# Kernel optimization log

Hardware: AMD Instinct MI355X
Metric: run time of the kernel (lower is better)

Reference implementation:

```python
import jax, jax.numpy as jnp
import numpy as np

IB = 8      # input/hidden activation bits
ABMVM = 8   # gate activation bits after MVM
ABNM = 8    # near-memory compute bits
NL = 0.05   # analog noise level
CY_DIV = 2.0
CY_SCALE = 2.0


def quant_pass(x, wb, sign):
    # Faithful port of QuantFunc.forward: clip/clamp then fake-quant (round to grid).
    if wb is None or wb == 0:
        return x
    if sign:
        delta = 0.0 if wb == 1 else 1.0 / (2.0 ** (wb - 1))
        x = jnp.clip(x, -1.0 + delta, 1.0 - delta)
    else:
        x = jnp.clip(x, 0.0, 1.0)
    if wb == 1:
        return jnp.sign(x)
    scale = 2.0 ** (wb - 1) if sign else 2.0 ** wb
    return jnp.round(x * scale) / scale


def setup_inputs() -> dict:
    key = jax.random.key(0)
    ks = jax.random.split(key, 7)
    B, I, H = 4096, 1024, 1024
    return {
        "input": jax.random.normal(ks[0], (B, I), jnp.float32),
        "hx": jax.random.normal(ks[1], (B, H), jnp.float32),
        "cx": jax.random.normal(ks[2], (B, H), jnp.float32),
        "weight_ih": jax.random.normal(ks[3], (4 * H, I), jnp.float32) * 0.1,
        "weight_hh": jax.random.normal(ks[4], (4 * H, H), jnp.float32) * 0.1,
        "bias_ih": jax.random.normal(ks[5], (4 * H,), jnp.float32) * 0.1,
        "bias_hh": jax.random.normal(ks[6], (4 * H,), jnp.float32) * 0.1,
        "train": 0,
    }


def reference(input, hx, cx, weight_ih, weight_hh, bias_ih, bias_hh, train):
    # Per-call Gaussian noise (simulated analog hardware); fixed key for reproducibility.
    nk = jax.random.split(jax.random.key(42), 4)
    noise_w_ih = jax.random.normal(nk[0], weight_ih.T.shape, weight_ih.dtype) * weight_ih.max() * NL
    noise_w_hh = jax.random.normal(nk[1], weight_hh.T.shape, weight_hh.dtype) * weight_hh.max() * NL
    noise_b_ih = jax.random.normal(nk[2], bias_ih.shape, bias_ih.dtype) * bias_ih.max() * NL
    noise_b_hh = jax.random.normal(nk[3], bias_hh.shape, bias_hh.dtype) * bias_hh.max() * NL

    # gates: [B, 4H]
    gates = (quant_pass(input, IB, True) @ (weight_ih.T + noise_w_ih) + bias_ih + noise_b_ih
             + quant_pass(hx, IB, True) @ (weight_hh.T + noise_w_hh) + bias_hh + noise_b_hh)

    ingate, forgetgate, cellgate, outgate = jnp.split(gates, 4, axis=1)
    ingate = quant_pass(jax.nn.sigmoid(ingate), ABMVM, False)
    forgetgate = quant_pass(jax.nn.sigmoid(forgetgate), ABMVM, False)
    cellgate = quant_pass(jnp.tanh(cellgate), ABMVM, True)
    outgate = quant_pass(jax.nn.sigmoid(outgate), ABMVM, False)

    cy = quant_pass((quant_pass(forgetgate * cx, ABNM, True)
                     + quant_pass(ingate * cellgate, ABNM, True)) / CY_DIV, ABNM, True)
    hy = quant_pass(outgate * quant_pass(jnp.tanh(cy * CY_SCALE), ABNM, True), ABNM, True)
    return (hy, cy)
```

## Files before the change

### kernel.cpp

```cpp
#include <hip/hip_runtime.h>
#include <hip/hip_bf16.h>
#include <stdint.h>
#include <stddef.h>


#define PART 1

typedef __attribute__((ext_vector_type(8))) short bf16x8;
typedef __attribute__((ext_vector_type(4))) float f32x4;

#define BATCH 4096

#define WS_A_OFF    ((size_t)0)
#define WS_B_OFF    ((size_t)16 << 20)
#define WS_G_OFF    ((size_t)48 << 20)
#define WS_BIAS_OFF ((size_t)112 << 20)
#define WS_MAX_OFF  (WS_BIAS_OFF + 16384)

__host__ __device__ inline void tf2x32(uint32_t k0, uint32_t k1,
                                       uint32_t x0, uint32_t x1,
                                       uint32_t &o0, uint32_t &o1)
{
  const uint32_t k2 = k0 ^ k1 ^ 0x1BD11BDAu;
#define TFR(r) { x0 += x1; x1 = (x1 << (r)) | (x1 >> (32 - (r))); x1 ^= x0; }
  x0 += k0; x1 += k1;
  TFR(13) TFR(15) TFR(26) TFR(6)
  x0 += k1; x1 += k2 + 1u;
  TFR(17) TFR(29) TFR(16) TFR(24)
  x0 += k2; x1 += k0 + 2u;
  TFR(13) TFR(15) TFR(26) TFR(6)
  x0 += k0; x1 += k1 + 3u;
  TFR(17) TFR(29) TFR(16) TFR(24)
  x0 += k1; x1 += k2 + 4u;
  TFR(13) TFR(15) TFR(26) TFR(6)
  x0 += k2; x1 += k0 + 5u;
#undef TFR
  o0 = x0; o1 = x1;
}

__device__ inline uint32_t jax_bits32(uint32_t k0, uint32_t k1, uint32_t i, uint32_t size)
{
#if PART
  uint32_t a, b;
  tf2x32(k0, k1, 0u, i, a, b);
  return a ^ b;
#else
  uint32_t half = size >> 1, a, b;
  if (i < half) { tf2x32(k0, k1, i, i + half, a, b); return a; }
  tf2x32(k0, k1, i - half, i, a, b); return b;
#endif
}

__device__ inline float bits_to_normal(uint32_t bits)
{
  float f = __uint_as_float((bits >> 9) | 0x3F800000u) - 1.0f;
  const float lo = -0x1.fffffep-1f;
  float u = fmaxf(lo, f * 2.0f + lo);
  float w = -log1pf(-u * u);
  float p;
  if (w < 5.0f) {
    w -= 2.5f;
    p = 2.81022636e-08f;
    p = fmaf(p, w, 3.43273939e-07f);
    p = fmaf(p, w, -3.5233877e-06f);
    p = fmaf(p, w, -4.39150654e-06f);
    p = fmaf(p, w, 0.00021858087f);
    p = fmaf(p, w, -0.00125372503f);
    p = fmaf(p, w, -0.00417768164f);
    p = fmaf(p, w, 0.246640727f);
    p = fmaf(p, w, 1.50140941f);
  } else {
    w = sqrtf(w) - 3.0f;
    p = -0.000200214257f;
    p = fmaf(p, w, 0.000100950558f);
    p = fmaf(p, w, 0.00134934322f);
    p = fmaf(p, w, -0.00367342844f);
    p = fmaf(p, w, 0.00573950773f);
    p = fmaf(p, w, -0.0076224613f);
    p = fmaf(p, w, 0.00943887047f);
    p = fmaf(p, w, 1.00167406f);
    p = fmaf(p, w, 2.83297682f);
  }
  return 0x1.6a09e6p+0f * (p * u);
}

__device__ inline float quantS8(float x)
{
  x = fminf(fmaxf(x, -0.9921875f), 0.9921875f);
  return rintf(x * 128.0f) * 0.0078125f;
}
__device__ inline float quantU8(float x)
{
  x = fminf(fmaxf(x, 0.0f), 1.0f);
  return rintf(x * 256.0f) * 0.00390625f;
}
__device__ inline float sigmoid_xla(float x) { return 0.5f + 0.5f * tanhf(0.5f * x); }

__device__ inline unsigned short f2bf(float x)
{
  uint32_t b = __float_as_uint(x);
  return (unsigned short)((b + 0x7FFFu + ((b >> 16) & 1u)) >> 16);
}
__device__ inline float bf2f(unsigned short u) { return __uint_as_float(((uint32_t)u) << 16); }

__device__ inline float dec_max(uint32_t u)
{
  uint32_t bits = (u & 0x80000000u) ? (u ^ 0x80000000u) : ~u;
  return __uint_as_float(bits);
}

__global__ void init_max(uint32_t* mx)
{
  if (threadIdx.x < 4) mx[threadIdx.x] = 0u;
}

__global__ void kmax(const float4* __restrict__ a, int n4, uint32_t* __restrict__ out)
{
  float m = -3.4e38f;
  for (int i = blockIdx.x * blockDim.x + threadIdx.x; i < n4; i += gridDim.x * blockDim.x) {
    float4 v = a[i];
    m = fmaxf(fmaxf(m, fmaxf(v.x, v.y)), fmaxf(v.z, v.w));
  }
  for (int off = 32; off; off >>= 1) m = fmaxf(m, __shfl_down(m, off, 64));
  __shared__ float sm[4];
  if ((threadIdx.x & 63) == 0) sm[threadIdx.x >> 6] = m;
  __syncthreads();
  if (threadIdx.x == 0) {
    float bm = sm[0];
    for (int w = 1; w < (int)(blockDim.x >> 6); ++w) bm = fmaxf(bm, sm[w]);
    uint32_t bits = __float_as_uint(bm);
    uint32_t enc = (bits & 0x80000000u) ? ~bits : (bits | 0x80000000u);
    atomicMax(out, enc);
  }
}

__global__ void build_A(const float4* __restrict__ in, const float4* __restrict__ hx,
                        unsigned short* __restrict__ A)
{
  int t = blockIdx.x * 256 + threadIdx.x;
  int b = t >> 9;
  int kq = t & 511;
  float4 v = (kq < 256) ? in[b * 256 + kq] : hx[b * 256 + (kq - 256)];
  unsigned short o[4];
  o[0] = f2bf(quantS8(v.x)); o[1] = f2bf(quantS8(v.y));
  o[2] = f2bf(quantS8(v.z)); o[3] = f2bf(quantS8(v.w));
  *reinterpret_cast<uint64_t*>(A + (size_t)t * 4) = *reinterpret_cast<uint64_t*>(o);
}

__global__ void build_B(const float* __restrict__ wih, const float* __restrict__ whh,
                        unsigned short* __restrict__ B, const uint32_t* __restrict__ mxenc,
                        uint32_t kih0, uint32_t kih1, uint32_t khh0, uint32_t khh1)
{
  uint32_t t = blockIdx.x * 256u + threadIdx.x;
  uint32_t arr = t >> 22;
  uint32_t r = t & 4194303u;
  uint32_t k = r & 1023u;
  uint32_t n = r >> 10;
  const float* w = arr ? whh : wih;
  float mx = dec_max(mxenc[arr]);
  uint32_t key0 = arr ? khh0 : kih0, key1 = arr ? khh1 : kih1;
  uint32_t i = k * 4096u + n;
  float nrm = bits_to_normal(jax_bits32(key0, key1, i, 4194304u));
  float weff = w[(size_t)n * 1024u + k] + (nrm * mx) * 0.05f;
  unsigned short hi = f2bf(weff);
  unsigned short lob = f2bf(weff - bf2f(hi));
  size_t base = (size_t)n * 4096u + (arr ? 1024u : 0u) + k;
  B[base] = hi;
  B[base + 2048u] = lob;
}

__global__ void build_bias(const float* __restrict__ bih, const float* __restrict__ bhh,
                           float* __restrict__ biasE, const uint32_t* __restrict__ mxenc,
                           uint32_t kbi0, uint32_t kbi1, uint32_t kbh0, uint32_t kbh1)
{
  uint32_t j = blockIdx.x * 256u + threadIdx.x;
  if (j >= 4096u) return;
  float mi = dec_max(mxenc[2]), mh = dec_max(mxenc[3]);
  float ni = (bits_to_normal(jax_bits32(kbi0, kbi1, j, 4096u)) * mi) * 0.05f;
  float nh = (bits_to_normal(jax_bits32(kbh0, kbh1, j, 4096u)) * mh) * 0.05f;
  biasE[j] = ((bih[j] + ni) + bhh[j]) + nh;
}


__device__ __forceinline__ void gload_lds16(const void* g, void* l)
{
  __builtin_amdgcn_global_load_lds((__attribute__((address_space(1))) void*)g,
                                   (__attribute__((address_space(3))) void*)l, 16, 0, 0);
}

#define VM4  asm volatile("s_waitcnt vmcnt(4)" ::: "memory")
#define VM0  asm volatile("s_waitcnt vmcnt(0)" ::: "memory")
#define NOVM

#define TILE_ONE(t_, DO_STAGE_, VM_ASM_)                                          \
  {                                                                               \
    const int buf_ = (t_) & 3;                                                    \
    const unsigned char* pa_ = lds + buf_ * 32768 + aoff;                         \
    const unsigned char* pb_ = lds + buf_ * 32768 + boff;                         \
    bf16x8 bfr_[4], af_[4];                                                       \
    _Pragma("unroll") for (int n_ = 0; n_ < 4; ++n_)                              \
      bfr_[n_] = *(const bf16x8*)(pb_ + n_ * 1024);                               \
    _Pragma("unroll") for (int m_ = 0; m_ < 4; ++m_)                              \
      af_[m_] = *(const bf16x8*)(pa_ + m_ * 1024);                                \
    if (DO_STAGE_) {                                                              \
      const int ts_ = (t_) + 2;                                                   \
      unsigned char* la_ = lds + (ts_ & 3) * 32768;                               \
      const int ka_ = (ts_ * 32) & 2047;                                          \
      gload_lds16(Ar0 + ka_, la_ + tid * 16);                                     \
      gload_lds16(Ar1 + ka_, la_ + 8192 + tid * 16);                              \
    }                                                                             \
    __builtin_amdgcn_s_barrier();                                                 \
    __builtin_amdgcn_sched_barrier(0);                                            \
    __builtin_amdgcn_s_setprio(1);                                                \
    _Pragma("unroll") for (int m_ = 0; m_ < 4; ++m_)                              \
      _Pragma("unroll") for (int n_ = 0; n_ < 4; ++n_)                            \
        acc[m_][n_] = __builtin_amdgcn_mfma_f32_16x16x32_bf16(af_[m_], bfr_[n_],  \
                                                              acc[m_][n_], 0, 0, 0); \
    __builtin_amdgcn_s_setprio(0);                                                \
    __builtin_amdgcn_s_barrier();                                                 \
    __builtin_amdgcn_sched_barrier(0);                                            \
    _Pragma("unroll") for (int m_ = 0; m_ < 4; ++m_)                              \
      af_[m_] = *(const bf16x8*)(pa_ + (4 + m_) * 1024);                          \
    if (DO_STAGE_) {                                                              \
      const int ts_ = (t_) + 2;                                                   \
      unsigned char* lb_ = lds + (ts_ & 3) * 32768 + 16384;                       \
      const size_t kb_ = (size_t)ts_ * 32;                                        \
      gload_lds16(Br0 + kb_, lb_ + tid * 16);                                     \
      gload_lds16(Br1 + kb_, lb_ + 8192 + tid * 16);                              \
    }                                                                             \
    __builtin_amdgcn_s_barrier();                                                 \
    __builtin_amdgcn_sched_barrier(0);                                            \
    __builtin_amdgcn_s_setprio(1);                                                \
    _Pragma("unroll") for (int m_ = 0; m_ < 4; ++m_)                              \
      _Pragma("unroll") for (int n_ = 0; n_ < 4; ++n_)                            \
        acc[4 + m_][n_] = __builtin_amdgcn_mfma_f32_16x16x32_bf16(af_[m_], bfr_[n_], \
                                                              acc[4 + m_][n_], 0, 0, 0); \
    __builtin_amdgcn_s_setprio(0);                                                \
    VM_ASM_;                                                                      \
    __builtin_amdgcn_s_barrier();                                                 \
    __builtin_amdgcn_sched_barrier(0);                                            \
  }

__global__ __launch_bounds__(512, 2) void gemm_gates(
    const unsigned short* __restrict__ A,
    const unsigned short* __restrict__ B,
    const float* __restrict__ bias,
    float* __restrict__ gates)
{
  extern __shared__ unsigned char lds[];
  const int tid  = threadIdx.x;
  const int lane = tid & 63;
  const int wave = tid >> 6;
  const int wr = wave >> 2;
  const int wc = wave & 3;

  const int bid = blockIdx.x;
  const int wg  = (bid & 7) * 32 + (bid >> 3);
  const int brow = (wg & 15) * 256;
  const int bcol = (wg >> 4) * 256;

  int sr0, sk0, sr1, sk1;
  {
    int c = tid, p = c >> 3, lc = (c & 7) ^ (p & 7);
    sr0 = p * 2 + (lc >> 2); sk0 = (lc & 3) * 8;
    c = tid + 512; p = c >> 3; lc = (c & 7) ^ (p & 7);
    sr1 = p * 2 + (lc >> 2); sk1 = (lc & 3) * 8;
  }
  const unsigned short* Ar0 = A + (size_t)(brow + sr0) * 2048 + sk0;
  const unsigned short* Ar1 = A + (size_t)(brow + sr1) * 2048 + sk1;
  const unsigned short* Br0 = B + (size_t)(bcol + sr0) * 4096 + sk0;
  const unsigned short* Br1 = B + (size_t)(bcol + sr1) * 4096 + sk1;

  const int lrh = (lane & 15) >> 1;
  const int chk = ((((lane & 1) << 2) | (lane >> 4)) ^ lrh);
  const int aoff = wr * 8192 + lrh * 128 + chk * 16;
  const int boff = 16384 + wc * 4096 + lrh * 128 + chk * 16;

  f32x4 acc[8][4] = {};

#pragma unroll
  for (int tt = 0; tt < 2; ++tt) {
    unsigned char* la = lds + tt * 32768;
    const int ka = tt * 32;
    gload_lds16(Ar0 + ka, la + tid * 16);
    gload_lds16(Ar1 + ka, la + 8192 + tid * 16);
    gload_lds16(Br0 + (size_t)(tt * 32), la + 16384 + tid * 16);
    gload_lds16(Br1 + (size_t)(tt * 32), la + 16384 + 8192 + tid * 16);
  }
  VM4;
  __builtin_amdgcn_s_barrier();
  __builtin_amdgcn_sched_barrier(0);

#pragma unroll 1
  for (int t = 0; t < 126; ++t) {
    TILE_ONE(t, 1, VM4);
  }
  TILE_ONE(126, 0, VM0);
  TILE_ONE(127, 0, NOVM);

  const int orow0 = brow + wr * 128 + ((lane >> 4) << 2);
  const int ocol0 = bcol + wc * 64 + (lane & 15);
#pragma unroll
  for (int n = 0; n < 4; ++n) {
    const int col = ocol0 + n * 16;
    const float bv = bias[col];
#pragma unroll
    for (int m = 0; m < 8; ++m) {
#pragma unroll
      for (int r = 0; r < 4; ++r)
        gates[(size_t)(orow0 + m * 16 + r) * 4096 + col] = acc[m][n][r] + bv;
    }
  }
}

__global__ void lstm_ew(const float* __restrict__ gates, const float* __restrict__ cx,
                        float* __restrict__ hy, float* __restrict__ cy)
{
  int idx = blockIdx.x * 256 + threadIdx.x;
  int b = idx >> 10, h = idx & 1023;
  const float* g = gates + (size_t)b * 4096;
  float ing = quantU8(sigmoid_xla(g[h]));
  float fg  = quantU8(sigmoid_xla(g[h + 1024]));
  float cg  = quantS8(tanhf(g[h + 2048]));
  float og  = quantU8(sigmoid_xla(g[h + 3072]));
  float c0  = cx[idx];
  float cyv = quantS8((quantS8(fg * c0) + quantS8(ing * cg)) * 0.5f);
  float hyv = quantS8(og * quantS8(tanhf(cyv * 2.0f)));
  hy[idx] = hyv;
  cy[idx] = cyv;
}

extern "C" void kernel_launch(void* const* d_in, const int* in_sizes, int n_in,
                              void* d_out, int out_size, void* d_ws, size_t ws_size,
                              hipStream_t stream)
{
  const float* input = (const float*)d_in[0];
  const float* hx    = (const float*)d_in[1];
  const float* cx    = (const float*)d_in[2];
  const float* wih   = (const float*)d_in[3];
  const float* whh   = (const float*)d_in[4];
  const float* bih   = (const float*)d_in[5];
  const float* bhh   = (const float*)d_in[6];
  (void)in_sizes; (void)n_in; (void)ws_size;

  uint8_t* ws = (uint8_t*)d_ws;
  unsigned short* A   = (unsigned short*)(ws + WS_A_OFF);
  unsigned short* B   = (unsigned short*)(ws + WS_B_OFF);
  float* gates        = (float*)(ws + WS_G_OFF);
  float* biasE        = (float*)(ws + WS_BIAS_OFF);
  uint32_t* mx        = (uint32_t*)(ws + WS_MAX_OFF);

  uint32_t nk[4][2];
#if PART
  for (int i = 0; i < 4; ++i) tf2x32(0u, 42u, 0u, (uint32_t)i, nk[i][0], nk[i][1]);
#else
  {
    uint32_t w0[4], w1[4];
    for (int i = 0; i < 4; ++i) tf2x32(0u, 42u, (uint32_t)i, (uint32_t)(i + 4), w0[i], w1[i]);
    uint32_t out8[8] = {w0[0], w0[1], w0[2], w0[3], w1[0], w1[1], w1[2], w1[3]};
    for (int i = 0; i < 4; ++i) { nk[i][0] = out8[2 * i]; nk[i][1] = out8[2 * i + 1]; }
  }
#endif

  init_max<<<1, 64, 0, stream>>>(mx);
  kmax<<<1024, 256, 0, stream>>>((const float4*)wih, 1048576, mx + 0);
  kmax<<<1024, 256, 0, stream>>>((const float4*)whh, 1048576, mx + 1);
  kmax<<<4, 256, 0, stream>>>((const float4*)bih, 1024, mx + 2);
  kmax<<<4, 256, 0, stream>>>((const float4*)bhh, 1024, mx + 3);

  build_A<<<8192, 256, 0, stream>>>((const float4*)input, (const float4*)hx, A);
  build_B<<<32768, 256, 0, stream>>>(wih, whh, B, mx, nk[0][0], nk[0][1], nk[1][0], nk[1][1]);
  build_bias<<<16, 256, 0, stream>>>(bih, bhh, biasE, mx, nk[2][0], nk[2][1], nk[3][0], nk[3][1]);

  (void)hipFuncSetAttribute((const void*)gemm_gates,
                            hipFuncAttributeMaxDynamicSharedMemorySize, 131072);
  gemm_gates<<<dim3(256), dim3(512), 131072, stream>>>(A, B, biasE, gates);

  float* hy = (float*)d_out;
  float* cyp = hy + (size_t)BATCH * 1024;
  lstm_ew<<<16384, 256, 0, stream>>>(gates, cx, hy, cyp);
}
```

Measured before the change: 233.6 us.

## Fuse LSTM elementwise epilogue into GEMM via interleaved gate columns

Permutes the B weight rows and bias so the four gates of each hidden unit sit in adjacent columns. The GEMM epilogue then stages its accumulator tile through LDS and computes the LSTM cell directly, writing hy and cy. This removes the 64 MB gates buffer round trip and the separate elementwise launch. The main loop is also simplified: both A halves are loaded up front, all four staging loads are issued together, and two of the per-tile barriers are removed, which raises register pressure and may change how loads overlap with MFMA.

```diff
diff --git a/kernel.cpp b/kernel.cpp
--- a/kernel.cpp
+++ b/kernel.cpp
@@ -13,8 +13,7 @@
 
 #define WS_A_OFF    ((size_t)0)
 #define WS_B_OFF    ((size_t)16 << 20)
-#define WS_G_OFF    ((size_t)48 << 20)
-#define WS_BIAS_OFF ((size_t)112 << 20)
+#define WS_BIAS_OFF ((size_t)48 << 20)
 #define WS_MAX_OFF  (WS_BIAS_OFF + 16384)
 
 __host__ __device__ inline void tf2x32(uint32_t k0, uint32_t k1,
@@ -164,7 +163,8 @@
   float weff = w[(size_t)n * 1024u + k] + (nrm * mx) * 0.05f;
   unsigned short hi = f2bf(weff);
   unsigned short lob = f2bf(weff - bf2f(hi));
-  size_t base = (size_t)n * 4096u + (arr ? 1024u : 0u) + k;
+  uint32_t np = (n & 1023u) * 4u + (n >> 10);
+  size_t base = (size_t)np * 4096u + (arr ? 1024u : 0u) + k;
   B[base] = hi;
   B[base + 2048u] = lob;
 }
@@ -178,9 +178,8 @@
   float mi = dec_max(mxenc[2]), mh = dec_max(mxenc[3]);
   float ni = (bits_to_normal(jax_bits32(kbi0, kbi1, j, 4096u)) * mi) * 0.05f;
   float nh = (bits_to_normal(jax_bits32(kbh0, kbh1, j, 4096u)) * mh) * 0.05f;
-  biasE[j] = ((bih[j] + ni) + bhh[j]) + nh;
-}
-
+  biasE[(j & 1023u) * 4u + (j >> 10)] = ((bih[j] + ni) + bhh[j]) + nh;
+}
 
 __device__ __forceinline__ void gload_lds16(const void* g, void* l)
 {
@@ -197,43 +196,31 @@
     const int buf_ = (t_) & 3;                                                    \
     const unsigned char* pa_ = lds + buf_ * 32768 + aoff;                         \
     const unsigned char* pb_ = lds + buf_ * 32768 + boff;                         \
-    bf16x8 bfr_[4], af_[4];                                                       \
+    bf16x8 bfr_[4], afL_[4], afH_[4];                                             \
     _Pragma("unroll") for (int n_ = 0; n_ < 4; ++n_)                              \
       bfr_[n_] = *(const bf16x8*)(pb_ + n_ * 1024);                               \
     _Pragma("unroll") for (int m_ = 0; m_ < 4; ++m_)                              \
-      af_[m_] = *(const bf16x8*)(pa_ + m_ * 1024);                                \
+      afL_[m_] = *(const bf16x8*)(pa_ + m_ * 1024);                               \
+    _Pragma("unroll") for (int m_ = 0; m_ < 4; ++m_)                              \
+      afH_[m_] = *(const bf16x8*)(pa_ + (4 + m_) * 1024);                         \
     if (DO_STAGE_) {                                                              \
       const int ts_ = (t_) + 2;                                                   \
       unsigned char* la_ = lds + (ts_ & 3) * 32768;                               \
       const int ka_ = (ts_ * 32) & 2047;                                          \
+      const size_t kb_ = (size_t)ts_ * 32;                                        \
       gload_lds16(Ar0 + ka_, la_ + tid * 16);                                     \
       gload_lds16(Ar1 + ka_, la_ + 8192 + tid * 16);                              \
+      gload_lds16(Br0 + kb_, la_ + 16384 + tid * 16);                             \
+      gload_lds16(Br1 + kb_, la_ + 16384 + 8192 + tid * 16);                      \
     }                                                                             \
-    __builtin_amdgcn_s_barrier();                                                 \
-    __builtin_amdgcn_sched_barrier(0);                                            \
     __builtin_amdgcn_s_setprio(1);                                                \
     _Pragma("unroll") for (int m_ = 0; m_ < 4; ++m_)                              \
       _Pragma("unroll") for (int n_ = 0; n_ < 4; ++n_)                            \
-        acc[m_][n_] = __builtin_amdgcn_mfma_f32_16x16x32_bf16(af_[m_], bfr_[n_],  \
+        acc[m_][n_] = __builtin_amdgcn_mfma_f32_16x16x32_bf16(afL_[m_], bfr_[n_], \
                                                               acc[m_][n_], 0, 0, 0); \
-    __builtin_amdgcn_s_setprio(0);                                                \
-    __builtin_amdgcn_s_barrier();                                                 \
-    __builtin_amdgcn_sched_barrier(0);                                            \
-    _Pragma("unroll") for (int m_ = 0; m_ < 4; ++m_)                              \
-      af_[m_] = *(const bf16x8*)(pa_ + (4 + m_) * 1024);                          \
-    if (DO_STAGE_) {                                                              \
-      const int ts_ = (t_) + 2;                                                   \
-      unsigned char* lb_ = lds + (ts_ & 3) * 32768 + 16384;                       \
-      const size_t kb_ = (size_t)ts_ * 32;                                        \
-      gload_lds16(Br0 + kb_, lb_ + tid * 16);                                     \
-      gload_lds16(Br1 + kb_, lb_ + 8192 + tid * 16);                              \
-    }                                                                             \
-    __builtin_amdgcn_s_barrier();                                                 \
-    __builtin_amdgcn_sched_barrier(0);                                            \
-    __builtin_amdgcn_s_setprio(1);                                                \
     _Pragma("unroll") for (int m_ = 0; m_ < 4; ++m_)                              \
       _Pragma("unroll") for (int n_ = 0; n_ < 4; ++n_)                            \
-        acc[4 + m_][n_] = __builtin_amdgcn_mfma_f32_16x16x32_bf16(af_[m_], bfr_[n_], \
+        acc[4 + m_][n_] = __builtin_amdgcn_mfma_f32_16x16x32_bf16(afH_[m_], bfr_[n_], \
                                                               acc[4 + m_][n_], 0, 0, 0); \
     __builtin_amdgcn_s_setprio(0);                                                \
     VM_ASM_;                                                                      \
@@ -245,7 +232,9 @@
     const unsigned short* __restrict__ A,
     const unsigned short* __restrict__ B,
     const float* __restrict__ bias,
-    float* __restrict__ gates)
+    const float* __restrict__ cx,
+    float* __restrict__ hy,
+    float* __restrict__ cy)
 {
   extern __shared__ unsigned char lds[];
   const int tid  = threadIdx.x;
@@ -298,36 +287,45 @@
   TILE_ONE(126, 0, VM0);
   TILE_ONE(127, 0, NOVM);
 
-  const int orow0 = brow + wr * 128 + ((lane >> 4) << 2);
-  const int ocol0 = bcol + wc * 64 + (lane & 15);
-#pragma unroll
-  for (int n = 0; n < 4; ++n) {
-    const int col = ocol0 + n * 16;
-    const float bv = bias[col];
-#pragma unroll
-    for (int m = 0; m < 8; ++m) {
-#pragma unroll
-      for (int r = 0; r < 4; ++r)
-        gates[(size_t)(orow0 + m * 16 + r) * 4096 + col] = acc[m][n][r] + bv;
+  float* LT = (float*)lds;
+  const int col_local0 = wc * 64 + (lane & 15);
+  const int lrow = (lane >> 4) << 2;
+  const int h = tid & 63;
+  const int hg = (bcol >> 2) + h;
+
+#pragma unroll
+  for (int hh = 0; hh < 2; ++hh) {
+    __syncthreads();
+#pragma unroll
+    for (int m = 0; m < 4; ++m) {
+#pragma unroll
+      for (int n = 0; n < 4; ++n) {
+        const int cl = col_local0 + n * 16;
+        const float bv = bias[bcol + cl];
+        const int lr0 = wr * 64 + m * 16 + lrow;
+#pragma unroll
+        for (int r = 0; r < 4; ++r)
+          LT[(lr0 + r) * 256 + cl] = acc[hh * 4 + m][n][r] + bv;
+      }
     }
-  }
-}
-
-__global__ void lstm_ew(const float* __restrict__ gates, const float* __restrict__ cx,
-                        float* __restrict__ hy, float* __restrict__ cy)
-{
-  int idx = blockIdx.x * 256 + threadIdx.x;
-  int b = idx >> 10, h = idx & 1023;
-  const float* g = gates + (size_t)b * 4096;
-  float ing = quantU8(sigmoid_xla(g[h]));
-  float fg  = quantU8(sigmoid_xla(g[h + 1024]));
-  float cg  = quantS8(tanhf(g[h + 2048]));
-  float og  = quantU8(sigmoid_xla(g[h + 3072]));
-  float c0  = cx[idx];
-  float cyv = quantS8((quantS8(fg * c0) + quantS8(ing * cg)) * 0.5f);
-  float hyv = quantS8(og * quantS8(tanhf(cyv * 2.0f)));
-  hy[idx] = hyv;
-  cy[idx] = cyv;
+    __syncthreads();
+#pragma unroll
+    for (int i = 0; i < 16; ++i) {
+      const int lr = (tid >> 6) * 16 + i;
+      const int grow = brow + ((lr >> 6) << 7) + hh * 64 + (lr & 63);
+      const float4 q = *(const float4*)(LT + lr * 256 + 4 * h);
+      const size_t oidx = (size_t)grow * 1024 + hg;
+      float ing = quantU8(sigmoid_xla(q.x));
+      float fg  = quantU8(sigmoid_xla(q.y));
+      float cg  = quantS8(tanhf(q.z));
+      float og  = quantU8(sigmoid_xla(q.w));
+      float c0  = cx[oidx];
+      float cyv = quantS8((quantS8(fg * c0) + quantS8(ing * cg)) * 0.5f);
+      float hyv = quantS8(og * quantS8(tanhf(cyv * 2.0f)));
+      hy[oidx] = hyv;
+      cy[oidx] = cyv;
+    }
+  }
 }
 
 extern "C" void kernel_launch(void* const* d_in, const int* in_sizes, int n_in,
@@ -346,7 +344,6 @@
   uint8_t* ws = (uint8_t*)d_ws;
   unsigned short* A   = (unsigned short*)(ws + WS_A_OFF);
   unsigned short* B   = (unsigned short*)(ws + WS_B_OFF);
-  float* gates        = (float*)(ws + WS_G_OFF);
   float* biasE        = (float*)(ws + WS_BIAS_OFF);
   uint32_t* mx        = (uint32_t*)(ws + WS_MAX_OFF);
 
@@ -372,11 +369,10 @@
   build_B<<<32768, 256, 0, stream>>>(wih, whh, B, mx, nk[0][0], nk[0][1], nk[1][0], nk[1][1]);
   build_bias<<<16, 256, 0, stream>>>(bih, bhh, biasE, mx, nk[2][0], nk[2][1], nk[3][0], nk[3][1]);
 
+  float* hy = (float*)d_out;
+  float* cyp = hy + (size_t)BATCH * 1024;
+
   (void)hipFuncSetAttribute((const void*)gemm_gates,
                             hipFuncAttributeMaxDynamicSharedMemorySize, 131072);
-  gemm_gates<<<dim3(256), dim3(512), 131072, stream>>>(A, B, biasE, gates);
-
-  float* hy = (float*)d_out;
-  float* cyp = hy + (size_t)BATCH * 1024;
-  lstm_ew<<<16384, 256, 0, stream>>>(gates, cx, hy, cyp);
-}
+  gemm_gates<<<dim3(256), dim3(512), 131072, stream>>>(A, B, biasE, cx, hy, cyp);
+}
```

After: 230.6 us. About the same (-1.3%).
